# Performance work log

Measured on AMD Instinct MI355X. Metric: run time of the kernel, lower is better.

Reference implementation:

```python
import jax, jax.numpy as jnp
import numpy as np

N = 50000      # nodes
E = 800000     # edges
D_IN = 128     # input_dim
NH = 64        # nhidden (per-head channels)
H = 2          # heads
TOP_K = 512
LN_EPS = 1e-5


def _ln(x, w, b):
    mu = x.mean(-1, keepdims=True)
    var = ((x - mu) ** 2).mean(-1, keepdims=True)
    return (x - mu) * jax.lax.rsqrt(var + LN_EPS) * w + b


def _gat_conv(x, edge_index, W, a_src, a_dst, bias):
    # PyG GATConv (concat=True, negative_slope=0.2, add_self_loops=True)
    n = x.shape[0]
    loops = jnp.arange(n, dtype=edge_index.dtype)
    src = jnp.concatenate([edge_index[0], loops])
    dst = jnp.concatenate([edge_index[1], loops])
    Hh, C = a_src.shape
    xp = (x @ W).reshape(n, Hh, C)                     # [N,H,C]
    al_s = (xp * a_src).sum(-1)                        # [N,H]
    al_d = (xp * a_dst).sum(-1)                        # [N,H]
    e = jax.nn.leaky_relu(al_s[src] + al_d[dst], 0.2)  # [E+N,H]
    m = jax.ops.segment_max(e, dst, num_segments=n)
    m = jnp.where(jnp.isfinite(m), m, 0.0)
    ex = jnp.exp(e - m[dst])
    denom = jax.ops.segment_sum(ex, dst, num_segments=n) + 1e-16
    alpha = ex / denom[dst]                            # scatter-softmax over dst
    out = jax.ops.segment_sum(alpha[:, :, None] * xp[src], dst, num_segments=n)
    return out.reshape(n, Hh * C) + bias


def setup_inputs() -> dict:
    key = jax.random.key(0)
    ks = jax.random.split(key, 16)
    p = lambda k, s: jax.random.normal(k, s, jnp.float32) * 0.05
    inp = {}
    inp["x1"] = jax.random.normal(ks[0], (N, D_IN), jnp.float32)
    inp["x2"] = jax.random.normal(ks[1], (N, D_IN), jnp.float32)
    inp["edge_index1"] = jax.random.randint(ks[2], (2, E), 0, N, jnp.int32)
    inp["edge_index2"] = jax.random.randint(ks[3], (2, E), 0, N, jnp.int32)
    # conv1: D_IN -> H*NH (concat)
    inp["W1"] = p(ks[4], (D_IN, H * NH))
    inp["as1"] = p(ks[5], (H, NH)); inp["ad1"] = p(ks[6], (H, NH))
    inp["b1"] = jnp.zeros((H * NH,), jnp.float32)
    # conv2: H*NH -> H*NH
    inp["W2"] = p(ks[7], (H * NH, H * NH))
    inp["as2"] = p(ks[8], (H, NH)); inp["ad2"] = p(ks[9], (H, NH))
    inp["b2"] = jnp.zeros((H * NH,), jnp.float32)
    # MLP head
    inp["fc1_w"] = p(ks[10], (TOP_K, 2 * NH)); inp["fc1_b"] = jnp.zeros((2 * NH,), jnp.float32)
    inp["ln1_w"] = jnp.ones((2 * NH,), jnp.float32); inp["ln1_b"] = jnp.zeros((2 * NH,), jnp.float32)
    inp["fc2_w"] = p(ks[11], (2 * NH, NH)); inp["fc2_b"] = jnp.zeros((NH,), jnp.float32)
    inp["ln2_w"] = jnp.ones((NH,), jnp.float32); inp["ln2_b"] = jnp.zeros((NH,), jnp.float32)
    inp["fc3_w"] = p(ks[12], (NH, 1)); inp["fc3_b"] = jnp.zeros((1,), jnp.float32)
    return inp


def _gnn(x, ei, W1, as1, ad1, b1, W2, as2, ad2, b2):
    h = jax.nn.relu(_gat_conv(x, ei, W1, as1, ad1, b1))
    return jax.nn.relu(_gat_conv(h, ei, W2, as2, ad2, b2))


def reference(x1, x2, edge_index1, edge_index2,
              W1, as1, ad1, b1, W2, as2, ad2, b2,
              fc1_w, fc1_b, ln1_w, ln1_b, fc2_w, fc2_b, ln2_w, ln2_b, fc3_w, fc3_b):
    out1 = _gnn(x1, edge_index1, W1, as1, ad1, b1, W2, as2, ad2, b2)
    out2 = _gnn(x2, edge_index2, W1, as1, ad1, b1, W2, as2, ad2, b2)
    # nn.PairwiseDistance(p=2, eps=1e-6): ||x1 - x2 + eps||_2 per row -> [N]
    diff = out1 - out2 + 1e-6
    sim = jnp.sqrt((diff * diff).sum(-1))
    topv, _ = jax.lax.top_k(sim, TOP_K)                # [TOP_K]
    h = jax.nn.relu(_ln(topv @ fc1_w + fc1_b, ln1_w, ln1_b))
    h = jax.nn.relu(_ln(h @ fc2_w + fc2_b, ln2_w, ln2_b))
    return jax.nn.sigmoid(h @ fc3_w + fc3_b)           # [1]
```

## Files before the change

kernel.cpp:

```cpp
#include <hip/hip_runtime.h>
#include <hip/hip_bf16.h>
#include <math.h>

#define N_NODES 50000
#define N_EDGES 800000
#define TOPK 512

__device__ __forceinline__ float lrelu02(float v) { return v > 0.f ? v : 0.2f * v; }

__device__ __forceinline__ unsigned short f2bf(float f) {
    unsigned u = __float_as_uint(f);
    u += 0x7fffu + ((u >> 16) & 1u);
    return (unsigned short)(u >> 16);
}

__global__ void k_count2(const int* __restrict__ ei1, const int* __restrict__ ei2,
                         int* __restrict__ cnt1, int* __restrict__ cnt2) {
    int e = blockIdx.x * 256 + threadIdx.x;
    if (e < N_EDGES) atomicAdd(&cnt1[ei1[N_EDGES + e]], 1);
    else if (e < 2 * N_EDGES) atomicAdd(&cnt2[ei2[e]], 1);
}

__global__ __launch_bounds__(1024) void k_scan1(const int* __restrict__ cnt1, const int* __restrict__ cnt2,
                                                int* __restrict__ rp1, int* __restrict__ rp2,
                                                int* __restrict__ part1, int* __restrict__ part2) {
    __shared__ int lds[1024];
    int g = blockIdx.y;
    const int* cnt = g ? cnt2 : cnt1;
    int* rp = g ? rp2 : rp1;
    int* part = g ? part2 : part1;
    int t = threadIdx.x;
    int i = blockIdx.x * 1024 + t;
    int v = (i < N_NODES) ? cnt[i] : 0;
    lds[t] = v;
    __syncthreads();
    for (int off = 1; off < 1024; off <<= 1) {
        int add = (t >= off) ? lds[t - off] : 0;
        __syncthreads();
        lds[t] += add;
        __syncthreads();
    }
    if (i < N_NODES) rp[i] = lds[t] - v;
    if (t == 1023) part[blockIdx.x] = lds[1023];
}

__global__ __launch_bounds__(128) void k_scan2(const int* __restrict__ part1, const int* __restrict__ part2,
                                               int* __restrict__ bo1, int* __restrict__ bo2,
                                               int* __restrict__ rp1, int* __restrict__ rp2) {
    int t = threadIdx.x, g = t >> 6, lane = t & 63;
    const int* part = g ? part2 : part1;
    int* bo = g ? bo2 : bo1;
    int v = (lane < 49) ? part[lane] : 0;
    int p = v;
    for (int d = 1; d < 64; d <<= 1) { int u = __shfl_up(p, d, 64); if (lane >= d) p += u; }
    if (lane < 49) bo[lane] = p - v;
    if (lane == 0) (g ? rp2 : rp1)[N_NODES] = N_EDGES;
}

__global__ __launch_bounds__(1024) void k_scan3(int* __restrict__ rp1, int* __restrict__ rp2,
                                                const int* __restrict__ bo1, const int* __restrict__ bo2) {
    int g = blockIdx.y;
    int* rp = g ? rp2 : rp1;
    int add = (g ? bo2 : bo1)[blockIdx.x];
    int i = blockIdx.x * 1024 + threadIdx.x;
    if (i < N_NODES) rp[i] += add;
}

__global__ void k_scatter2(const int* __restrict__ ei1, const int* __restrict__ ei2,
                           const int* __restrict__ rp1, const int* __restrict__ rp2,
                           int* __restrict__ cur1, int* __restrict__ cur2,
                           int* __restrict__ ssrc1, int* __restrict__ ssrc2) {
    int e = blockIdx.x * 256 + threadIdx.x;
    if (e < N_EDGES) {
        int src = ei1[e], dst = ei1[N_EDGES + e];
        ssrc1[rp1[dst] + atomicAdd(&cur1[dst], 1)] = src;
    } else if (e < 2 * N_EDGES) {
        int ee = e - N_EDGES;
        int src = ei2[ee], dst = ei2[e];
        ssrc2[rp2[dst] + atomicAdd(&cur2[dst], 1)] = src;
    }
}

template<int IN_BF16>
__global__ __launch_bounds__(256) void k_gemm_att(
    const void* __restrict__ XA_, const void* __restrict__ XB_, const float* __restrict__ W,
    const float* __restrict__ a_src, const float* __restrict__ a_dst,
    unsigned short* __restrict__ YA, unsigned short* __restrict__ YB,
    float2* __restrict__ alsA, float2* __restrict__ aldA,
    float2* __restrict__ alsB, float2* __restrict__ aldB) {
    __shared__ __align__(16) float Xs[64][128];
    __shared__ __align__(16) float Wl[128][64];
    int t = threadIdx.x;
    int head = blockIdx.y;
    int row0 = blockIdx.x * 64;
    const void* X = blockIdx.z ? XB_ : XA_;
    unsigned short* Y = blockIdx.z ? YB : YA;
    float* als = (float*)(blockIdx.z ? alsB : alsA);
    float* ald = (float*)(blockIdx.z ? aldB : aldA);

    const float4* W4 = (const float4*)W;
    float4* Wl4 = (float4*)Wl;
    #pragma unroll
    for (int i = 0; i < 8; ++i) {
        int e = i * 256 + t;
        int k = e >> 4, cc = e & 15;
        Wl4[k * 16 + cc] = W4[k * 32 + head * 16 + cc];
    }
    float4* Xs4 = (float4*)Xs;
    if (IN_BF16) {
        const uint4* Xb = (const uint4*)X;
        #pragma unroll
        for (int i = 0; i < 4; ++i) {
            int e = i * 256 + t;
            int r = e >> 4, c8 = e & 15;
            int g = row0 + r;
            uint4 v = make_uint4(0u, 0u, 0u, 0u);
            if (g < N_NODES) v = Xb[g * 16 + c8];
            float4 f0 = make_float4(__uint_as_float(v.x << 16), __uint_as_float(v.x & 0xffff0000u),
                                    __uint_as_float(v.y << 16), __uint_as_float(v.y & 0xffff0000u));
            float4 f1 = make_float4(__uint_as_float(v.z << 16), __uint_as_float(v.z & 0xffff0000u),
                                    __uint_as_float(v.w << 16), __uint_as_float(v.w & 0xffff0000u));
            int c0 = c8 * 2, c1 = c0 + 1;
            Xs4[r * 32 + ((c0 + r + (r >> 2)) & 31)] = f0;
            Xs4[r * 32 + ((c1 + r + (r >> 2)) & 31)] = f1;
        }
    } else {
        const float4* X4 = (const float4*)X;
        #pragma unroll
        for (int i = 0; i < 8; ++i) {
            int e = i * 256 + t;
            int r = e >> 5, c = e & 31;
            int g = row0 + r;
            float4 v = make_float4(0.f, 0.f, 0.f, 0.f);
            if (g < N_NODES) v = X4[(size_t)g * 32 + c];
            int ch = (c + r + (r >> 2)) & 31;
            Xs4[r * 32 + ch] = v;
        }
    }
    __syncthreads();

    int tc = t & 15, tr = t >> 4;
    int r0 = tr * 4;
    float acc[4][4];
    #pragma unroll
    for (int r = 0; r < 4; ++r)
        #pragma unroll
        for (int c = 0; c < 4; ++c) acc[r][c] = 0.f;

    for (int k = 0; k < 128; k += 4) {
        int kc = k >> 2;
        float4 w0 = *(const float4*)&Wl[k][tc * 4];
        float4 w1 = *(const float4*)&Wl[k + 1][tc * 4];
        float4 w2 = *(const float4*)&Wl[k + 2][tc * 4];
        float4 w3 = *(const float4*)&Wl[k + 3][tc * 4];
        #pragma unroll
        for (int r = 0; r < 4; ++r) {
            int row = r0 + r;
            int ch = (kc + row + (row >> 2)) & 31;
            float4 xv = Xs4[row * 32 + ch];
            acc[r][0] += xv.x * w0.x + xv.y * w1.x + xv.z * w2.x + xv.w * w3.x;
            acc[r][1] += xv.x * w0.y + xv.y * w1.y + xv.z * w2.y + xv.w * w3.y;
            acc[r][2] += xv.x * w0.z + xv.y * w1.z + xv.z * w2.z + xv.w * w3.z;
            acc[r][3] += xv.x * w0.w + xv.y * w1.w + xv.z * w2.w + xv.w * w3.w;
        }
    }

    float s0 = a_src[head * 64 + tc * 4 + 0], s1 = a_src[head * 64 + tc * 4 + 1];
    float s2 = a_src[head * 64 + tc * 4 + 2], s3 = a_src[head * 64 + tc * 4 + 3];
    float d0 = a_dst[head * 64 + tc * 4 + 0], d1 = a_dst[head * 64 + tc * 4 + 1];
    float d2 = a_dst[head * 64 + tc * 4 + 2], d3 = a_dst[head * 64 + tc * 4 + 3];

    #pragma unroll
    for (int r = 0; r < 4; ++r) {
        int g = row0 + r0 + r;
        float ps = acc[r][0] * s0 + acc[r][1] * s1 + acc[r][2] * s2 + acc[r][3] * s3;
        float pd = acc[r][0] * d0 + acc[r][1] * d1 + acc[r][2] * d2 + acc[r][3] * d3;
        #pragma unroll
        for (int m = 1; m < 16; m <<= 1) {
            ps += __shfl_xor(ps, m, 64);
            pd += __shfl_xor(pd, m, 64);
        }
        if (g < N_NODES) {
            ushort4 pk;
            pk.x = f2bf(acc[r][0]); pk.y = f2bf(acc[r][1]);
            pk.z = f2bf(acc[r][2]); pk.w = f2bf(acc[r][3]);
            *(ushort4*)&Y[(size_t)g * 128 + head * 64 + tc * 4] = pk;
            if (tc == 0) { als[g * 2 + head] = ps; ald[g * 2 + head] = pd; }
        }
    }
}

__device__ __forceinline__ void agg4(
    const unsigned short* __restrict__ xp, const float2* __restrict__ als2,
    const float2* __restrict__ ald2, const int* __restrict__ rp,
    const int* __restrict__ ssrc, int node, int lane, float* r ) {
    const uint4* xp4 = (const uint4*)xp;
    int lg = lane & 15, grp = lane >> 4;
    float2 adv = ald2[node];
    float2 asf = als2[node];
    float ws0 = __expf(lrelu02(asf.x + adv.x));
    float ws1 = __expf(lrelu02(asf.y + adv.y));
    float a0 = 0.f, a1 = 0.f, a2 = 0.f, a3 = 0.f, a4 = 0.f, a5 = 0.f, a6 = 0.f, a7 = 0.f;
    float dp0 = 0.f, dp1 = 0.f;
    int start = rp[node], end = rp[node + 1];
    for (int j0 = start; j0 < end; j0 += 64) {
        int rem = end - j0;
        int sv = 0; float w0v = 0.f, w1v = 0.f;
        if (lane < rem) {
            sv = ssrc[j0 + lane];
            float2 a = als2[sv];
            w0v = __expf(lrelu02(a.x + adv.x));
            w1v = __expf(lrelu02(a.y + adv.y));
        }
        dp0 += w0v; dp1 += w1v;
        int len = rem < 64 ? rem : 64;
        int nit = (len + 3) >> 2;
        int i = 0;
        for (; i + 2 <= nit; i += 2) {
            int la = 4 * i + grp, lb = la + 4;
            int sa = __shfl(sv, la, 64);
            int sb = __shfl(sv, lb, 64);
            float wa0 = __shfl(w0v, la, 64), wa1 = __shfl(w1v, la, 64);
            float wb0 = __shfl(w0v, lb, 64), wb1 = __shfl(w1v, lb, 64);
            uint4 va = xp4[sa * 16 + lg];
            uint4 vb = xp4[sb * 16 + lg];
            float wa = (lg >= 8) ? wa1 : wa0;
            float wb = (lg >= 8) ? wb1 : wb0;
            a0 = fmaf(wa, __uint_as_float(va.x << 16), a0);
            a1 = fmaf(wa, __uint_as_float(va.x & 0xffff0000u), a1);
            a2 = fmaf(wa, __uint_as_float(va.y << 16), a2);
            a3 = fmaf(wa, __uint_as_float(va.y & 0xffff0000u), a3);
            a4 = fmaf(wa, __uint_as_float(va.z << 16), a4);
            a5 = fmaf(wa, __uint_as_float(va.z & 0xffff0000u), a5);
            a6 = fmaf(wa, __uint_as_float(va.w << 16), a6);
            a7 = fmaf(wa, __uint_as_float(va.w & 0xffff0000u), a7);
            a0 = fmaf(wb, __uint_as_float(vb.x << 16), a0);
            a1 = fmaf(wb, __uint_as_float(vb.x & 0xffff0000u), a1);
            a2 = fmaf(wb, __uint_as_float(vb.y << 16), a2);
            a3 = fmaf(wb, __uint_as_float(vb.y & 0xffff0000u), a3);
            a4 = fmaf(wb, __uint_as_float(vb.z << 16), a4);
            a5 = fmaf(wb, __uint_as_float(vb.z & 0xffff0000u), a5);
            a6 = fmaf(wb, __uint_as_float(vb.w << 16), a6);
            a7 = fmaf(wb, __uint_as_float(vb.w & 0xffff0000u), a7);
        }
        if (i < nit) {
            int la = 4 * i + grp;
            int sa = __shfl(sv, la, 64);
            float wa0 = __shfl(w0v, la, 64), wa1 = __shfl(w1v, la, 64);
            uint4 va = xp4[sa * 16 + lg];
            float wa = (lg >= 8) ? wa1 : wa0;
            a0 = fmaf(wa, __uint_as_float(va.x << 16), a0);
            a1 = fmaf(wa, __uint_as_float(va.x & 0xffff0000u), a1);
            a2 = fmaf(wa, __uint_as_float(va.y << 16), a2);
            a3 = fmaf(wa, __uint_as_float(va.y & 0xffff0000u), a3);
            a4 = fmaf(wa, __uint_as_float(va.z << 16), a4);
            a5 = fmaf(wa, __uint_as_float(va.z & 0xffff0000u), a5);
            a6 = fmaf(wa, __uint_as_float(va.w << 16), a6);
            a7 = fmaf(wa, __uint_as_float(va.w & 0xffff0000u), a7);
        }
    }
    #pragma unroll
    for (int m = 16; m < 64; m <<= 1) {
        a0 += __shfl_xor(a0, m, 64); a1 += __shfl_xor(a1, m, 64);
        a2 += __shfl_xor(a2, m, 64); a3 += __shfl_xor(a3, m, 64);
        a4 += __shfl_xor(a4, m, 64); a5 += __shfl_xor(a5, m, 64);
        a6 += __shfl_xor(a6, m, 64); a7 += __shfl_xor(a7, m, 64);
    }
    #pragma unroll
    for (int m = 1; m < 64; m <<= 1) {
        dp0 += __shfl_xor(dp0, m, 64);
        dp1 += __shfl_xor(dp1, m, 64);
    }
    uint4 v = xp4[node * 16 + lg];
    float wss = (lg >= 8) ? ws1 : ws0;
    a0 = fmaf(wss, __uint_as_float(v.x << 16), a0);
    a1 = fmaf(wss, __uint_as_float(v.x & 0xffff0000u), a1);
    a2 = fmaf(wss, __uint_as_float(v.y << 16), a2);
    a3 = fmaf(wss, __uint_as_float(v.y & 0xffff0000u), a3);
    a4 = fmaf(wss, __uint_as_float(v.z << 16), a4);
    a5 = fmaf(wss, __uint_as_float(v.z & 0xffff0000u), a5);
    a6 = fmaf(wss, __uint_as_float(v.w << 16), a6);
    a7 = fmaf(wss, __uint_as_float(v.w & 0xffff0000u), a7);
    float inv = 1.f / (((lg >= 8) ? dp1 + ws1 : dp0 + ws0) + 1e-16f);
    r[0] = a0 * inv; r[1] = a1 * inv; r[2] = a2 * inv; r[3] = a3 * inv;
    r[4] = a4 * inv; r[5] = a5 * inv; r[6] = a6 * inv; r[7] = a7 * inv;
}

__global__ __launch_bounds__(256) void k_agg_l1(
    const unsigned short* __restrict__ xpA, const float2* __restrict__ alsA, const float2* __restrict__ aldA,
    const int* __restrict__ rp1, const int* __restrict__ ssrc1, unsigned short* __restrict__ tmpA,
    const unsigned short* __restrict__ xpB, const float2* __restrict__ alsB, const float2* __restrict__ aldB,
    const int* __restrict__ rp2, const int* __restrict__ ssrc2, unsigned short* __restrict__ tmpB,
    const float* __restrict__ bias) {
    int g = blockIdx.y;
    const unsigned short* xp = g ? xpB : xpA;
    const float2* als = g ? alsB : alsA;
    const float2* ald = g ? aldB : aldA;
    const int* rp = g ? rp2 : rp1;
    const int* ssrc = g ? ssrc2 : ssrc1;
    unsigned short* out = g ? tmpB : tmpA;
    int node = blockIdx.x * 4 + (threadIdx.x >> 6);
    int lane = threadIdx.x & 63;
    int lg = lane & 15;
    float r[8];
    agg4(xp, als, ald, rp, ssrc, node, lane, r);
    float4 b0 = *(const float4*)&bias[8 * lg];
    float4 b1 = *(const float4*)&bias[8 * lg + 4];
    float o0 = fmaxf(r[0] + b0.x, 0.f), o1 = fmaxf(r[1] + b0.y, 0.f);
    float o2 = fmaxf(r[2] + b0.z, 0.f), o3 = fmaxf(r[3] + b0.w, 0.f);
    float o4 = fmaxf(r[4] + b1.x, 0.f), o5 = fmaxf(r[5] + b1.y, 0.f);
    float o6 = fmaxf(r[6] + b1.z, 0.f), o7 = fmaxf(r[7] + b1.w, 0.f);
    if ((lane >> 4) == 0) {
        uint4 o;
        o.x = (unsigned)f2bf(o0) | ((unsigned)f2bf(o1) << 16);
        o.y = (unsigned)f2bf(o2) | ((unsigned)f2bf(o3) << 16);
        o.z = (unsigned)f2bf(o4) | ((unsigned)f2bf(o5) << 16);
        o.w = (unsigned)f2bf(o6) | ((unsigned)f2bf(o7) << 16);
        ((uint4*)out)[node * 16 + lg] = o;
    }
}

__global__ __launch_bounds__(256) void k_agg_l2(
    const unsigned short* __restrict__ xpA, const float2* __restrict__ alsA, const float2* __restrict__ aldA,
    const int* __restrict__ rp1, const int* __restrict__ ssrc1,
    const unsigned short* __restrict__ xpB, const float2* __restrict__ alsB, const float2* __restrict__ aldB,
    const int* __restrict__ rp2, const int* __restrict__ ssrc2,
    const float* __restrict__ bias, float* __restrict__ sim, int* __restrict__ hist) {
    int node = blockIdx.x * 4 + (threadIdx.x >> 6);
    int lane = threadIdx.x & 63;
    int lg = lane & 15;
    float ra[8], rb[8];
    agg4(xpA, alsA, aldA, rp1, ssrc1, node, lane, ra);
    agg4(xpB, alsB, aldB, rp2, ssrc2, node, lane, rb);
    float4 b0 = *(const float4*)&bias[8 * lg];
    float4 b1 = *(const float4*)&bias[8 * lg + 4];
    float bb[8] = {b0.x, b0.y, b0.z, b0.w, b1.x, b1.y, b1.z, b1.w};
    float p = 0.f;
    #pragma unroll
    for (int i = 0; i < 8; ++i) {
        float av = fmaxf(ra[i] + bb[i], 0.f);
        float bv = fmaxf(rb[i] + bb[i], 0.f);
        float d = av - bv + 1e-6f;
        p = fmaf(d, d, p);
    }
    #pragma unroll
    for (int m = 1; m < 16; m <<= 1) p += __shfl_xor(p, m, 64);
    if (lane == 0) {
        float sv = sqrtf(p);
        sim[node] = sv;
        atomicAdd(&hist[__float_as_uint(sv) >> 16], 1);
    }
}

__global__ __launch_bounds__(1024) void k_select2(
    const float* __restrict__ sim, const int* __restrict__ hhi,
    int* __restrict__ hlo, int* __restrict__ state) {
    __shared__ int lds[1024];
    __shared__ int sbin, scnt;
    int t = threadIdx.x;
    int base = t * 64;
    int local = 0;
    for (int i = 0; i < 64; ++i) local += hhi[base + i];
    lds[t] = local;
    __syncthreads();
    for (int off = 1; off < 1024; off <<= 1) {
        int add = (t + off < 1024) ? lds[t + off] : 0;
        __syncthreads();
        lds[t] += add;
        __syncthreads();
    }
    int incl = lds[t];
    int above = (t < 1023) ? lds[t + 1] : 0;
    if (above < TOPK && incl >= TOPK) {
        int c = above;
        for (int b = 63; b >= 0; --b) {
            int h = hhi[base + b];
            if (c + h >= TOPK) { sbin = base + b; scnt = c; break; }
            c += h;
        }
    }
    __syncthreads();
    int hb = sbin, cA = scnt;
    for (int i = t; i < N_NODES; i += 1024) {
        unsigned key = __float_as_uint(sim[i]);
        if ((int)(key >> 16) == hb) atomicAdd(&hlo[key & 0xFFFF], 1);
    }
    __threadfence();
    __syncthreads();
    int K2 = TOPK - cA;
    local = 0;
    for (int i = 0; i < 64; ++i) local += hlo[base + i];
    lds[t] = local;
    __syncthreads();
    for (int off = 1; off < 1024; off <<= 1) {
        int add = (t + off < 1024) ? lds[t + off] : 0;
        __syncthreads();
        lds[t] += add;
        __syncthreads();
    }
    incl = lds[t];
    above = (t < 1023) ? lds[t + 1] : 0;
    if (above < K2 && incl >= K2) {
        int c = above;
        for (int b = 63; b >= 0; --b) {
            int h = hlo[base + b];
            if (c + h >= K2) {
                state[2] = (int)((((unsigned)hb) << 16) | (unsigned)(base + b));
                state[3] = cA + c;
                break;
            }
            c += h;
        }
    }
}

__global__ __launch_bounds__(512) void k_sort_mlp(
    const float* __restrict__ sim, const int* __restrict__ state,
    const float* __restrict__ fc1_w, const float* __restrict__ fc1_b,
    const float* __restrict__ ln1_w, const float* __restrict__ ln1_b,
    const float* __restrict__ fc2_w, const float* __restrict__ fc2_b,
    const float* __restrict__ ln2_w, const float* __restrict__ ln2_b,
    const float* __restrict__ fc3_w, const float* __restrict__ fc3_b,
    float* __restrict__ outp) {
    __shared__ float s[512];
    __shared__ float h1p[4][128];
    __shared__ float h1[128];
    __shared__ float h2[64];
    __shared__ float stats[2];
    __shared__ int cnt;
    int t = threadIdx.x;
    unsigned T = (unsigned)state[2];
    int nG = state[3];
    if (t == 0) cnt = 0;
    __syncthreads();
    for (int i = t; i < N_NODES; i += 512) {
        float v = sim[i];
        if (__float_as_uint(v) > T) { int p = atomicAdd(&cnt, 1); s[p] = v; }
    }
    __syncthreads();
    if (t >= nG) s[t] = __uint_as_float(T);
    __syncthreads();
    for (int k = 2; k <= 512; k <<= 1)
        for (int j = k >> 1; j > 0; j >>= 1) {
            int ixj = t ^ j;
            if (ixj > t) {
                float a = s[t], b = s[ixj];
                bool up = ((t & k) == 0);
                if ((a > b) == up) { s[t] = b; s[ixj] = a; }
            }
            __syncthreads();
        }
    {
        int o = t & 127, seg = t >> 7;
        float acc = 0.f;
        for (int i = seg * 128; i < seg * 128 + 128; ++i)
            acc += s[511 - i] * fc1_w[i * 128 + o];
        h1p[seg][o] = acc;
    }
    __syncthreads();
    if (t < 128) h1[t] = fc1_b[t] + h1p[0][t] + h1p[1][t] + h1p[2][t] + h1p[3][t];
    __syncthreads();
    if (t == 0) {
        float mu = 0.f;
        for (int i = 0; i < 128; ++i) mu += h1[i];
        mu *= (1.f / 128.f);
        float var = 0.f;
        for (int i = 0; i < 128; ++i) { float d = h1[i] - mu; var += d * d; }
        var *= (1.f / 128.f);
        stats[0] = mu; stats[1] = rsqrtf(var + 1e-5f);
    }
    __syncthreads();
    if (t < 128) h1[t] = fmaxf((h1[t] - stats[0]) * stats[1] * ln1_w[t] + ln1_b[t], 0.f);
    __syncthreads();
    if (t < 64) {
        float acc = fc2_b[t];
        for (int i = 0; i < 128; ++i) acc += h1[i] * fc2_w[i * 64 + t];
        h2[t] = acc;
    }
    __syncthreads();
    if (t == 0) {
        float mu = 0.f;
        for (int i = 0; i < 64; ++i) mu += h2[i];
        mu *= (1.f / 64.f);
        float var = 0.f;
        for (int i = 0; i < 64; ++i) { float d = h2[i] - mu; var += d * d; }
        var *= (1.f / 64.f);
        stats[0] = mu; stats[1] = rsqrtf(var + 1e-5f);
    }
    __syncthreads();
    if (t < 64) h2[t] = fmaxf((h2[t] - stats[0]) * stats[1] * ln2_w[t] + ln2_b[t], 0.f);
    __syncthreads();
    if (t == 0) {
        float z = fc3_b[0];
        for (int i = 0; i < 64; ++i) z += h2[i] * fc3_w[i];
        outp[0] = 1.f / (1.f + expf(-z));
    }
}

extern "C" void kernel_launch(void* const* d_in, const int* in_sizes, int n_in,
                              void* d_out, int out_size, void* d_ws, size_t ws_size,
                              hipStream_t stream) {
    const float* x1 = (const float*)d_in[0];
    const float* x2 = (const float*)d_in[1];
    const int* ei1 = (const int*)d_in[2];
    const int* ei2 = (const int*)d_in[3];
    const float* W1 = (const float*)d_in[4];
    const float* as1 = (const float*)d_in[5];
    const float* ad1 = (const float*)d_in[6];
    const float* b1 = (const float*)d_in[7];
    const float* W2 = (const float*)d_in[8];
    const float* as2 = (const float*)d_in[9];
    const float* ad2 = (const float*)d_in[10];
    const float* b2 = (const float*)d_in[11];
    const float* fc1_w = (const float*)d_in[12];
    const float* fc1_b = (const float*)d_in[13];
    const float* ln1_w = (const float*)d_in[14];
    const float* ln1_b = (const float*)d_in[15];
    const float* fc2_w = (const float*)d_in[16];
    const float* fc2_b = (const float*)d_in[17];
    const float* ln2_w = (const float*)d_in[18];
    const float* ln2_b = (const float*)d_in[19];
    const float* fc3_w = (const float*)d_in[20];
    const float* fc3_b = (const float*)d_in[21];
    float* outp = (float*)d_out;

    char* ws = (char*)d_ws;
    size_t off = 0;
    auto alloc = [&](size_t bytes) -> void* {
        void* p = ws + off;
        off = (off + bytes + 255) & ~(size_t)255;
        return p;
    };
    unsigned short* xpA = (unsigned short*)alloc((size_t)N_NODES * 128 * 2);
    unsigned short* xpB = (unsigned short*)alloc((size_t)N_NODES * 128 * 2);
    unsigned short* tmpA = (unsigned short*)alloc((size_t)N_NODES * 128 * 2);
    unsigned short* tmpB = (unsigned short*)alloc((size_t)N_NODES * 128 * 2);
    int* ssrc1  = (int*)alloc((size_t)N_EDGES * 4);
    int* ssrc2  = (int*)alloc((size_t)N_EDGES * 4);
    int* rp1    = (int*)alloc((size_t)(N_NODES + 1) * 4);
    int* rp2    = (int*)alloc((size_t)(N_NODES + 1) * 4);
    float2* alsA = (float2*)alloc((size_t)N_NODES * 8);
    float2* aldA = (float2*)alloc((size_t)N_NODES * 8);
    float2* alsB = (float2*)alloc((size_t)N_NODES * 8);
    float2* aldB = (float2*)alloc((size_t)N_NODES * 8);
    int* part1 = (int*)alloc(64 * 4);
    int* part2 = (int*)alloc(64 * 4);
    int* bo1   = (int*)alloc(64 * 4);
    int* bo2   = (int*)alloc(64 * 4);
    float* sim = (float*)alloc((size_t)N_NODES * 4);
    char* zbase = ws + off;
    int* cnt1 = (int*)alloc((size_t)N_NODES * 4);
    int* cnt2 = (int*)alloc((size_t)N_NODES * 4);
    int* cur1 = (int*)alloc((size_t)N_NODES * 4);
    int* cur2 = (int*)alloc((size_t)N_NODES * 4);
    int* hist1 = (int*)alloc(65536 * 4);
    int* hist2 = (int*)alloc(65536 * 4);
    int* state = (int*)alloc(64);
    size_t zsize = (size_t)((ws + off) - zbase);
    hipMemsetAsync(zbase, 0, zsize, stream);

    k_count2<<<6250, 256, 0, stream>>>(ei1, ei2, cnt1, cnt2);
    k_scan1<<<dim3(49, 2), 1024, 0, stream>>>(cnt1, cnt2, rp1, rp2, part1, part2);
    k_scan2<<<1, 128, 0, stream>>>(part1, part2, bo1, bo2, rp1, rp2);
    k_scan3<<<dim3(49, 2), 1024, 0, stream>>>(rp1, rp2, bo1, bo2);
    k_scatter2<<<6250, 256, 0, stream>>>(ei1, ei2, rp1, rp2, cur1, cur2, ssrc1, ssrc2);

    dim3 ggrid(782, 2, 2);
    k_gemm_att<0><<<ggrid, 256, 0, stream>>>(x1, x2, W1, as1, ad1, xpA, xpB, alsA, aldA, alsB, aldB);
    k_agg_l1<<<dim3(12500, 2), 256, 0, stream>>>(xpA, alsA, aldA, rp1, ssrc1, tmpA,
                                                 xpB, alsB, aldB, rp2, ssrc2, tmpB, b1);
    k_gemm_att<1><<<ggrid, 256, 0, stream>>>(tmpA, tmpB, W2, as2, ad2,
                                             xpA, xpB, alsA, aldA, alsB, aldB);
    k_agg_l2<<<12500, 256, 0, stream>>>(xpA, alsA, aldA, rp1, ssrc1,
                                        xpB, alsB, aldB, rp2, ssrc2, b2, sim, hist1);

    k_select2<<<1, 1024, 0, stream>>>(sim, hist1, hist2, state);
    k_sort_mlp<<<1, 512, 0, stream>>>(sim, state, fc1_w, fc1_b, ln1_w, ln1_b,
                                      fc2_w, fc2_b, ln2_w, ln2_b, fc3_w, fc3_b, outp);
}
```

Baseline: 805.9 us.

## Remap aggregation blocks per XCD by graph and split layer-2 distance into own kernel

The aggregation kernel now uses a 1D grid whose block index is decoded so each group of four XCDs (by blockIdx mod 8) works on only one graph. The aim is to keep each XCD's L2 cache holding a single graph's features and CSR data. Layer 2 reuses this kernel instead of aggregating both graphs in one block, writing bf16 outputs that a new small kernel reads to compute pairwise distance and the histogram. This adds a kernel launch and an extra round trip through memory, and the layer-2 outputs are rounded to bf16 before the distance is computed, which slightly changes precision.

```diff
diff --git a/kernel.cpp b/kernel.cpp
--- a/kernel.cpp
+++ b/kernel.cpp
@@ -286,20 +286,23 @@
     r[4] = a4 * inv; r[5] = a5 * inv; r[6] = a6 * inv; r[7] = a7 * inv;
 }
 
-__global__ __launch_bounds__(256) void k_agg_l1(
+__global__ __launch_bounds__(256) void k_agg(
     const unsigned short* __restrict__ xpA, const float2* __restrict__ alsA, const float2* __restrict__ aldA,
-    const int* __restrict__ rp1, const int* __restrict__ ssrc1, unsigned short* __restrict__ tmpA,
+    const int* __restrict__ rp1, const int* __restrict__ ssrc1, unsigned short* __restrict__ outA,
     const unsigned short* __restrict__ xpB, const float2* __restrict__ alsB, const float2* __restrict__ aldB,
-    const int* __restrict__ rp2, const int* __restrict__ ssrc2, unsigned short* __restrict__ tmpB,
+    const int* __restrict__ rp2, const int* __restrict__ ssrc2, unsigned short* __restrict__ outB,
     const float* __restrict__ bias) {
-    int g = blockIdx.y;
+    int x = blockIdx.x;
+    int xcd = x & 7;
+    int g = xcd >> 2;
+    int j = (x >> 3) * 4 + (xcd & 3);
     const unsigned short* xp = g ? xpB : xpA;
     const float2* als = g ? alsB : alsA;
     const float2* ald = g ? aldB : aldA;
     const int* rp = g ? rp2 : rp1;
     const int* ssrc = g ? ssrc2 : ssrc1;
-    unsigned short* out = g ? tmpB : tmpA;
-    int node = blockIdx.x * 4 + (threadIdx.x >> 6);
+    unsigned short* out = g ? outB : outA;
+    int node = j * 4 + (threadIdx.x >> 6);
     int lane = threadIdx.x & 63;
     int lg = lane & 15;
     float r[8];
@@ -320,32 +323,29 @@
     }
 }
 
-__global__ __launch_bounds__(256) void k_agg_l2(
-    const unsigned short* __restrict__ xpA, const float2* __restrict__ alsA, const float2* __restrict__ aldA,
-    const int* __restrict__ rp1, const int* __restrict__ ssrc1,
-    const unsigned short* __restrict__ xpB, const float2* __restrict__ alsB, const float2* __restrict__ aldB,
-    const int* __restrict__ rp2, const int* __restrict__ ssrc2,
-    const float* __restrict__ bias, float* __restrict__ sim, int* __restrict__ hist) {
-    int node = blockIdx.x * 4 + (threadIdx.x >> 6);
-    int lane = threadIdx.x & 63;
-    int lg = lane & 15;
-    float ra[8], rb[8];
-    agg4(xpA, alsA, aldA, rp1, ssrc1, node, lane, ra);
-    agg4(xpB, alsB, aldB, rp2, ssrc2, node, lane, rb);
-    float4 b0 = *(const float4*)&bias[8 * lg];
-    float4 b1 = *(const float4*)&bias[8 * lg + 4];
-    float bb[8] = {b0.x, b0.y, b0.z, b0.w, b1.x, b1.y, b1.z, b1.w};
+__global__ __launch_bounds__(256) void k_dist(
+    const unsigned short* __restrict__ outA, const unsigned short* __restrict__ outB,
+    float* __restrict__ sim, int* __restrict__ hist) {
+    int t = threadIdx.x;
+    int node = blockIdx.x * 16 + (t >> 4);
+    int lg = t & 15;
+    uint4 va = ((const uint4*)outA)[node * 16 + lg];
+    uint4 vb = ((const uint4*)outB)[node * 16 + lg];
     float p = 0.f;
-    #pragma unroll
-    for (int i = 0; i < 8; ++i) {
-        float av = fmaxf(ra[i] + bb[i], 0.f);
-        float bv = fmaxf(rb[i] + bb[i], 0.f);
-        float d = av - bv + 1e-6f;
-        p = fmaf(d, d, p);
+    {
+        float d;
+        d = __uint_as_float(va.x << 16)         - __uint_as_float(vb.x << 16)         + 1e-6f; p = fmaf(d, d, p);
+        d = __uint_as_float(va.x & 0xffff0000u) - __uint_as_float(vb.x & 0xffff0000u) + 1e-6f; p = fmaf(d, d, p);
+        d = __uint_as_float(va.y << 16)         - __uint_as_float(vb.y << 16)         + 1e-6f; p = fmaf(d, d, p);
+        d = __uint_as_float(va.y & 0xffff0000u) - __uint_as_float(vb.y & 0xffff0000u) + 1e-6f; p = fmaf(d, d, p);
+        d = __uint_as_float(va.z << 16)         - __uint_as_float(vb.z << 16)         + 1e-6f; p = fmaf(d, d, p);
+        d = __uint_as_float(va.z & 0xffff0000u) - __uint_as_float(vb.z & 0xffff0000u) + 1e-6f; p = fmaf(d, d, p);
+        d = __uint_as_float(va.w << 16)         - __uint_as_float(vb.w << 16)         + 1e-6f; p = fmaf(d, d, p);
+        d = __uint_as_float(va.w & 0xffff0000u) - __uint_as_float(vb.w & 0xffff0000u) + 1e-6f; p = fmaf(d, d, p);
     }
     #pragma unroll
     for (int m = 1; m < 16; m <<= 1) p += __shfl_xor(p, m, 64);
-    if (lane == 0) {
+    if (lg == 0) {
         float sv = sqrtf(p);
         sim[node] = sv;
         atomicAdd(&hist[__float_as_uint(sv) >> 16], 1);
@@ -567,12 +567,13 @@
 
     dim3 ggrid(782, 2, 2);
     k_gemm_att<0><<<ggrid, 256, 0, stream>>>(x1, x2, W1, as1, ad1, xpA, xpB, alsA, aldA, alsB, aldB);
-    k_agg_l1<<<dim3(12500, 2), 256, 0, stream>>>(xpA, alsA, aldA, rp1, ssrc1, tmpA,
-                                                 xpB, alsB, aldB, rp2, ssrc2, tmpB, b1);
+    k_agg<<<25000, 256, 0, stream>>>(xpA, alsA, aldA, rp1, ssrc1, tmpA,
+                                     xpB, alsB, aldB, rp2, ssrc2, tmpB, b1);
     k_gemm_att<1><<<ggrid, 256, 0, stream>>>(tmpA, tmpB, W2, as2, ad2,
                                              xpA, xpB, alsA, aldA, alsB, aldB);
-    k_agg_l2<<<12500, 256, 0, stream>>>(xpA, alsA, aldA, rp1, ssrc1,
-                                        xpB, alsB, aldB, rp2, ssrc2, b2, sim, hist1);
+    k_agg<<<25000, 256, 0, stream>>>(xpA, alsA, aldA, rp1, ssrc1, tmpA,
+                                     xpB, alsB, aldB, rp2, ssrc2, tmpB, b2);
+    k_dist<<<3125, 256, 0, stream>>>(tmpA, tmpB, sim, hist1);
 
     k_select2<<<1, 1024, 0, stream>>>(sim, hist1, hist2, state);
     k_sort_mlp<<<1, 512, 0, stream>>>(sim, state, fc1_w, fc1_b, ln1_w, ln1_b,
```

Measured after the change: 810.2 us. Within noise of the previous version (+0.5%).
